# Kernel tuning notes

Hardware: AMD Instinct MI355X
Metric: run time of the kernel (lower is better)

The kernel has to match this reference:

```python
import jax, jax.numpy as jnp
import numpy as np

EPS = 1e-6

def _layernorm(x, g, b):
    mu = jnp.mean(x, axis=-1, keepdims=True)
    var = jnp.mean(jnp.square(x - mu), axis=-1, keepdims=True)
    return (x - mu) * jax.lax.rsqrt(var + EPS) * g + b

def setup_inputs() -> dict:
    key = jax.random.key(0)
    ks = jax.random.split(key, 5)
    B, S, C = 8, 4096, 2048
    M = 2048  # mid_channels must equal channels (norm2 shape constraint)
    x = jax.random.normal(ks[0], (B, S, C), dtype=jnp.float32)
    w1 = jax.random.normal(ks[1], (C, M), dtype=jnp.float32) * (1.0 / np.sqrt(C))
    b1 = jnp.zeros((M,), dtype=jnp.float32)
    w2 = jax.random.normal(ks[2], (M, C), dtype=jnp.float32) * (1.0 / np.sqrt(M))
    b2 = jnp.zeros((C,), dtype=jnp.float32)
    g1 = jnp.ones((C,), dtype=jnp.float32)
    be1 = jnp.zeros((C,), dtype=jnp.float32)
    g2 = jnp.ones((M,), dtype=jnp.float32)
    be2 = jnp.zeros((M,), dtype=jnp.float32)
    return {"x": x, "w1": w1, "b1": b1, "w2": w2, "b2": b2,
            "g1": g1, "be1": be1, "g2": g2, "be2": be2}

def reference(x, w1, b1, w2, b2, g1, be1, g2, be2):
    h = _layernorm(x, g1, be1)
    h = jax.nn.silu(h)
    h = jnp.einsum('bsc,cm->bsm', h, w1) + b1
    h = _layernorm(h, g2, be2)
    h = jax.nn.silu(h)
    # dropout is identity in eval mode
    h = jnp.einsum('bsm,mc->bsc', h, w2) + b2
    return x + h
```

## Files before the change

### kernel.cpp

```cpp
#include <hip/hip_runtime.h>
#include <hip/hip_bf16.h>
#include <stdint.h>

#define NROWS 32768
#define KDIM  2048
#define MDIM  2048

typedef __attribute__((ext_vector_type(8))) __bf16 bf16x8;
typedef __attribute__((ext_vector_type(4))) __bf16 bf16x4;
typedef __attribute__((ext_vector_type(4))) float  f32x4;

__device__ __forceinline__ void gload16(const __bf16* g, __bf16* l) {
    __builtin_amdgcn_global_load_lds(
        (__attribute__((address_space(1))) void*)(g),
        (__attribute__((address_space(3))) void*)(l), 16, 0, 0);
}

__global__ __launch_bounds__(256) void wsplit(const float* __restrict__ W,
                                              __bf16* __restrict__ th,
                                              __bf16* __restrict__ tl) {
    __shared__ float tile[32][33];
    const int bx = blockIdx.x & 63;
    const int by = blockIdx.x >> 6;
    const int tx = threadIdx.x & 31;
    const int ty = threadIdx.x >> 5;
#pragma unroll
    for (int i = 0; i < 32; i += 8)
        tile[ty + i][tx] = W[(size_t)(by * 32 + ty + i) * MDIM + bx * 32 + tx];
    __syncthreads();
#pragma unroll
    for (int i = 0; i < 32; i += 8) {
        const int m = bx * 32 + ty + i;
        const int k = by * 32 + tx;
        const float v = tile[tx][ty + i];
        const __bf16 hb = (__bf16)v;
        const __bf16 lb = (__bf16)(v - (float)hb);
        th[(size_t)m * KDIM + k] = hb;
        tl[(size_t)m * KDIM + k] = lb;
    }
}

__global__ __launch_bounds__(256) void ln_silu(const float* __restrict__ in,
                                               const float* __restrict__ g,
                                               const float* __restrict__ beta,
                                               __bf16* __restrict__ hi) {
    const int row  = blockIdx.x;
    const int tid  = threadIdx.x;
    const int lane = tid & 63;
    const int wv   = tid >> 6;
    const float* rp = in + (size_t)row * KDIM;

    const float4 v0 = ((const float4*)rp)[tid];
    const float4 v1 = ((const float4*)rp)[tid + 256];

    float s = v0.x + v0.y + v0.z + v0.w + v1.x + v1.y + v1.z + v1.w;
    float q = v0.x * v0.x + v0.y * v0.y + v0.z * v0.z + v0.w * v0.w +
              v1.x * v1.x + v1.y * v1.y + v1.z * v1.z + v1.w * v1.w;

#pragma unroll
    for (int off = 32; off > 0; off >>= 1) {
        s += __shfl_xor(s, off, 64);
        q += __shfl_xor(q, off, 64);
    }
    __shared__ float red[8];
    if (lane == 0) { red[wv] = s; red[4 + wv] = q; }
    __syncthreads();
    s = red[0] + red[1] + red[2] + red[3];
    q = red[4] + red[5] + red[6] + red[7];

    const float mu   = s * (1.0f / KDIM);
    const float var  = q * (1.0f / KDIM) - mu * mu;
    const float rstd = rsqrtf(var + 1e-6f);

    auto emit = [&](float4 v, int c0) {
        bf16x4 h4;
        const float xs[4] = {v.x, v.y, v.z, v.w};
#pragma unroll
        for (int j = 0; j < 4; j++) {
            const int c = c0 + j;
            const float t  = (xs[j] - mu) * rstd * g[c] + beta[c];
            const float sv = t / (1.0f + __expf(-t));
            h4[j] = (__bf16)sv;
        }
        *(bf16x4*)(hi + (size_t)row * KDIM + c0) = h4;
    };
    emit(v0, tid * 4);
    emit(v1, 1024 + tid * 4);
}

#define PB   8192
#define BOFF 24576
#define NT   (KDIM / 32)

#define MM(ACC, A_, H_, L_)                                                    \
    ACC = __builtin_amdgcn_mfma_f32_16x16x32_bf16(A_, H_, ACC, 0, 0, 0);       \
    ACC = __builtin_amdgcn_mfma_f32_16x16x32_bf16(A_, L_, ACC, 0, 0, 0)

#define PHASE_PRE()                                                            \
    __builtin_amdgcn_s_barrier();                                              \
    asm volatile("s_waitcnt lgkmcnt(0)" ::: "memory");                         \
    __builtin_amdgcn_sched_barrier(0);                                         \
    __builtin_amdgcn_s_setprio(1)

#define PHASE_POST()                                                           \
    __builtin_amdgcn_s_setprio(0);                                             \
    __builtin_amdgcn_s_barrier()

__global__ __launch_bounds__(512, 2) void gemm8p(
        const __bf16* __restrict__ Ah,
        const __bf16* __restrict__ Bh, const __bf16* __restrict__ Bl,
        const float* __restrict__ bias, const float* __restrict__ res,
        float* __restrict__ out) {
    __shared__ __align__(16) __bf16 lds[57344];

    const int tid  = threadIdx.x;
    const int lane = tid & 63;
    const int wv   = tid >> 6;
    const int wr   = wv >> 2;
    const int wc   = wv & 3;
    const int ml   = lane & 15;
    const int qk   = lane >> 4;

    const int bid = blockIdx.x;
    const int g   = (bid & 7) * 128 + (bid >> 3);
    const int m0  = (g & 127) * 256;
    const int n0  = (g >> 7) * 256;

    const int srow = wv * 16 + (lane >> 2);
    const int scol = ((lane & 3) ^ ((lane >> 3) & 3)) * 8;
    const __bf16* pA0 = Ah + (size_t)(m0 + srow) * KDIM + scol;
    const __bf16* pA1 = Ah + (size_t)(m0 + 128 + srow) * KDIM + scol;
    const __bf16* pH0 = Bh + (size_t)(n0 + srow) * KDIM + scol;
    const __bf16* pH1 = Bh + (size_t)(n0 + 128 + srow) * KDIM + scol;
    const __bf16* pL0 = Bl + (size_t)(n0 + srow) * KDIM + scol;
    const __bf16* pL1 = Bl + (size_t)(n0 + 128 + srow) * KDIM + scol;
    const int ld0 = wv * 512;
    const int ld1 = 4096 + wv * 512;

    const int cofs = (qk ^ ((ml >> 1) & 3)) * 8;
    const int aoff = (wr * 128 + ml) * 32 + cofs;
    const int boff = (wc * 64 + ml) * 32 + cofs;

    f32x4 acc[8][4] = {};

    gload16(pH0, lds + BOFF + ld0);
    gload16(pH1, lds + BOFF + ld1);
    gload16(pL0, lds + BOFF + PB + ld0);
    gload16(pL1, lds + BOFF + PB + ld1);
    gload16(pA0, lds + ld0);
    gload16(pA1, lds + ld1);
    gload16(pA0 + 32, lds + PB + ld0);
    gload16(pA1 + 32, lds + PB + ld1);
    asm volatile("s_waitcnt vmcnt(2)" ::: "memory");
    __builtin_amdgcn_sched_barrier(0);
    __builtin_amdgcn_s_barrier();

    int ta = 0;
    int pa = 2;
    for (int t = 0; t < NT; ++t) {
        __bf16* const aB = lds + ta * PB;
        __bf16* const hB = lds + BOFF + (t & 1) * 2 * PB;
        __bf16* const lB = hB + PB;
        __bf16* const hN = lds + BOFF + ((t + 1) & 1) * 2 * PB;
        const bool pfB = (t + 1) < NT;
        const bool pfA = (t + 2) < NT;
        const int  kB  = (t + 1) * 32;
        const int  kA  = (t + 2) * 32;

        bf16x8 a0, a1, a2, a3, h0, h1, h2, h3, l0, l1, l2, l3;

        a0 = *(const bf16x8*)(aB + aoff);
        a1 = *(const bf16x8*)(aB + aoff + 512);
        a2 = *(const bf16x8*)(aB + aoff + 1024);
        a3 = *(const bf16x8*)(aB + aoff + 1536);
        h0 = *(const bf16x8*)(hB + boff);
        h1 = *(const bf16x8*)(hB + boff + 512);
        l0 = *(const bf16x8*)(lB + boff);
        l1 = *(const bf16x8*)(lB + boff + 512);
        if (pfB) {
            gload16(pH0 + kB, hN + ld0);
            gload16(pH1 + kB, hN + ld1);
        }
        PHASE_PRE();
        MM(acc[0][0], a0, h0, l0); MM(acc[1][0], a1, h0, l0);
        MM(acc[2][0], a2, h0, l0); MM(acc[3][0], a3, h0, l0);
        MM(acc[0][1], a0, h1, l1); MM(acc[1][1], a1, h1, l1);
        MM(acc[2][1], a2, h1, l1); MM(acc[3][1], a3, h1, l1);
        PHASE_POST();

        h2 = *(const bf16x8*)(hB + boff + 1024);
        h3 = *(const bf16x8*)(hB + boff + 1536);
        l2 = *(const bf16x8*)(lB + boff + 1024);
        l3 = *(const bf16x8*)(lB + boff + 1536);
        if (pfB) {
            gload16(pL0 + kB, hN + PB + ld0);
            gload16(pL1 + kB, hN + PB + ld1);
        }
        PHASE_PRE();
        MM(acc[0][2], a0, h2, l2); MM(acc[1][2], a1, h2, l2);
        MM(acc[2][2], a2, h2, l2); MM(acc[3][2], a3, h2, l2);
        MM(acc[0][3], a0, h3, l3); MM(acc[1][3], a1, h3, l3);
        MM(acc[2][3], a2, h3, l3); MM(acc[3][3], a3, h3, l3);
        PHASE_POST();

        a0 = *(const bf16x8*)(aB + aoff + 2048);
        a1 = *(const bf16x8*)(aB + aoff + 2560);
        a2 = *(const bf16x8*)(aB + aoff + 3072);
        a3 = *(const bf16x8*)(aB + aoff + 3584);
        if (pfA) {
            gload16(pA0 + kA, lds + pa * PB + ld0);
            gload16(pA1 + kA, lds + pa * PB + ld1);
        }
        PHASE_PRE();
        MM(acc[4][2], a0, h2, l2); MM(acc[5][2], a1, h2, l2);
        MM(acc[6][2], a2, h2, l2); MM(acc[7][2], a3, h2, l2);
        MM(acc[4][3], a0, h3, l3); MM(acc[5][3], a1, h3, l3);
        MM(acc[6][3], a2, h3, l3); MM(acc[7][3], a3, h3, l3);
        PHASE_POST();

        PHASE_PRE();
        MM(acc[4][0], a0, h0, l0); MM(acc[5][0], a1, h0, l0);
        MM(acc[6][0], a2, h0, l0); MM(acc[7][0], a3, h0, l0);
        MM(acc[4][1], a0, h1, l1); MM(acc[5][1], a1, h1, l1);
        MM(acc[6][1], a2, h1, l1); MM(acc[7][1], a3, h1, l1);
        __builtin_amdgcn_s_setprio(0);
        if (pfA) {
            asm volatile("s_waitcnt vmcnt(2)" ::: "memory");
        } else if (pfB) {
            asm volatile("s_waitcnt vmcnt(0)" ::: "memory");
        }
        __builtin_amdgcn_sched_barrier(0);
        if (pfB) __builtin_amdgcn_s_barrier();

        ta = (ta == 2) ? 0 : ta + 1;
        pa = (pa == 2) ? 0 : pa + 1;
    }

#pragma unroll
    for (int i = 0; i < 8; i++) {
        const int gm = m0 + wr * 128 + (i >> 2) * 64 + (i & 3) * 16 + qk * 4;
#pragma unroll
        for (int j = 0; j < 4; j++) {
            const int gn = n0 + wc * 64 + j * 16 + ml;
            const float bv = bias[gn];
#pragma unroll
            for (int r = 0; r < 4; r++) {
                const size_t idx = (size_t)(gm + r) * MDIM + gn;
                float v = acc[i][j][r] + bv;
                if (res) v += res[idx];
                out[idx] = v;
            }
        }
    }
}

extern "C" void kernel_launch(void* const* d_in, const int* in_sizes, int n_in,
                              void* d_out, int out_size, void* d_ws, size_t ws_size,
                              hipStream_t stream) {
    const float* x   = (const float*)d_in[0];
    const float* w1  = (const float*)d_in[1];
    const float* b1  = (const float*)d_in[2];
    const float* w2  = (const float*)d_in[3];
    const float* b2  = (const float*)d_in[4];
    const float* g1  = (const float*)d_in[5];
    const float* be1 = (const float*)d_in[6];
    const float* g2  = (const float*)d_in[7];
    const float* be2 = (const float*)d_in[8];
    float* out = (float*)d_out;

    char* ws = (char*)d_ws;
    const size_t PLANE = (size_t)NROWS * KDIM * 2;
    const size_t WPL   = (size_t)KDIM * MDIM * 2;
    __bf16* Ahp = (__bf16*)(ws);
    __bf16* B1h = (__bf16*)(ws + PLANE);
    __bf16* B1l = (__bf16*)(ws + PLANE + WPL);
    __bf16* B2h = (__bf16*)(ws + PLANE + 2 * WPL);
    __bf16* B2l = (__bf16*)(ws + PLANE + 3 * WPL);

    wsplit<<<4096, 256, 0, stream>>>(w1, B1h, B1l);
    wsplit<<<4096, 256, 0, stream>>>(w2, B2h, B2l);

    ln_silu<<<NROWS, 256, 0, stream>>>(x, g1, be1, Ahp);
    gemm8p<<<(NROWS / 256) * (MDIM / 256), 512, 0, stream>>>(
        Ahp, B1h, B1l, b1, nullptr, out);

    ln_silu<<<NROWS, 256, 0, stream>>>(out, g2, be2, Ahp);
    gemm8p<<<(NROWS / 256) * (MDIM / 256), 512, 0, stream>>>(
        Ahp, B2h, B2l, b2, x, out);
}
```

Measured before the change: 1.654 ms.

## Replace 8-phase ping-pong GEMM schedule with single-phase load-all-then-compute loop

Removes the four intra-iteration barrier/setprio phases that interleaved LDS fragment reads, global prefetches and MFMA groups. Each K-step now reads all A and B fragments into registers up front, issues every prefetch, then runs all 64 MFMAs under raised priority with a single barrier at the end. This cuts the number of block barriers per iteration, but it raises register pressure and loses the fine-grained overlap between LDS reads and MFMA work across the two co-resident waves.

```diff
diff --git a/kernel.cpp b/kernel.cpp
--- a/kernel.cpp
+++ b/kernel.cpp
@@ -88,7 +88,8 @@
     emit(v1, 1024 + tid * 4);
 }
 
-#define PB   8192
+#define PB_A 8192
+#define PB_B 8192
 #define BOFF 24576
 #define NT   (KDIM / 32)
 
@@ -96,17 +97,7 @@
     ACC = __builtin_amdgcn_mfma_f32_16x16x32_bf16(A_, H_, ACC, 0, 0, 0);       \
     ACC = __builtin_amdgcn_mfma_f32_16x16x32_bf16(A_, L_, ACC, 0, 0, 0)
 
-#define PHASE_PRE()                                                            \
-    __builtin_amdgcn_s_barrier();                                              \
-    asm volatile("s_waitcnt lgkmcnt(0)" ::: "memory");                         \
-    __builtin_amdgcn_sched_barrier(0);                                         \
-    __builtin_amdgcn_s_setprio(1)
-
-#define PHASE_POST()                                                           \
-    __builtin_amdgcn_s_setprio(0);                                             \
-    __builtin_amdgcn_s_barrier()
-
-__global__ __launch_bounds__(512, 2) void gemm8p(
+__global__ __launch_bounds__(512, 2) void gemmtp(
         const __bf16* __restrict__ Ah,
         const __bf16* __restrict__ Bh, const __bf16* __restrict__ Bl,
         const float* __restrict__ bias, const float* __restrict__ res,
@@ -145,95 +136,88 @@
 
     gload16(pH0, lds + BOFF + ld0);
     gload16(pH1, lds + BOFF + ld1);
-    gload16(pL0, lds + BOFF + PB + ld0);
-    gload16(pL1, lds + BOFF + PB + ld1);
+    gload16(pL0, lds + BOFF + PB_B + ld0);
+    gload16(pL1, lds + BOFF + PB_B + ld1);
     gload16(pA0, lds + ld0);
     gload16(pA1, lds + ld1);
-    gload16(pA0 + 32, lds + PB + ld0);
-    gload16(pA1 + 32, lds + PB + ld1);
+    gload16(pA0 + 32, lds + PB_A + ld0);
+    gload16(pA1 + 32, lds + PB_A + ld1);
     asm volatile("s_waitcnt vmcnt(2)" ::: "memory");
     __builtin_amdgcn_sched_barrier(0);
     __builtin_amdgcn_s_barrier();
+    __builtin_amdgcn_sched_barrier(0);
 
     int ta = 0;
-    int pa = 2;
     for (int t = 0; t < NT; ++t) {
-        __bf16* const aB = lds + ta * PB;
-        __bf16* const hB = lds + BOFF + (t & 1) * 2 * PB;
-        __bf16* const lB = hB + PB;
-        __bf16* const hN = lds + BOFF + ((t + 1) & 1) * 2 * PB;
+        __bf16* const aCur = lds + ta * PB_A;
+        const int tan_ = (ta == 2) ? 0 : ta + 1;
+        const int pa_  = (tan_ == 2) ? 0 : tan_ + 1;
+        __bf16* const bCur = lds + BOFF + ((t & 1) ? 2 * PB_B : 0);
+        __bf16* const bNxt = lds + BOFF + ((t & 1) ? 0 : 2 * PB_B);
         const bool pfB = (t + 1) < NT;
         const bool pfA = (t + 2) < NT;
-        const int  kB  = (t + 1) * 32;
-        const int  kA  = (t + 2) * 32;
-
-        bf16x8 a0, a1, a2, a3, h0, h1, h2, h3, l0, l1, l2, l3;
-
-        a0 = *(const bf16x8*)(aB + aoff);
-        a1 = *(const bf16x8*)(aB + aoff + 512);
-        a2 = *(const bf16x8*)(aB + aoff + 1024);
-        a3 = *(const bf16x8*)(aB + aoff + 1536);
-        h0 = *(const bf16x8*)(hB + boff);
-        h1 = *(const bf16x8*)(hB + boff + 512);
-        l0 = *(const bf16x8*)(lB + boff);
-        l1 = *(const bf16x8*)(lB + boff + 512);
+
+        bf16x8 aL[4], aH[4], hB[4], lB[4];
+        aL[0] = *(const bf16x8*)(aCur + aoff);
+        aL[1] = *(const bf16x8*)(aCur + aoff + 512);
+        aL[2] = *(const bf16x8*)(aCur + aoff + 1024);
+        aL[3] = *(const bf16x8*)(aCur + aoff + 1536);
+        hB[0] = *(const bf16x8*)(bCur + boff);
+        hB[1] = *(const bf16x8*)(bCur + boff + 512);
+        hB[2] = *(const bf16x8*)(bCur + boff + 1024);
+        hB[3] = *(const bf16x8*)(bCur + boff + 1536);
+        lB[0] = *(const bf16x8*)(bCur + PB_B + boff);
+        lB[1] = *(const bf16x8*)(bCur + PB_B + boff + 512);
+        lB[2] = *(const bf16x8*)(bCur + PB_B + boff + 1024);
+        lB[3] = *(const bf16x8*)(bCur + PB_B + boff + 1536);
+        aH[0] = *(const bf16x8*)(aCur + aoff + 2048);
+        aH[1] = *(const bf16x8*)(aCur + aoff + 2560);
+        aH[2] = *(const bf16x8*)(aCur + aoff + 3072);
+        aH[3] = *(const bf16x8*)(aCur + aoff + 3584);
+
         if (pfB) {
-            gload16(pH0 + kB, hN + ld0);
-            gload16(pH1 + kB, hN + ld1);
-        }
-        PHASE_PRE();
-        MM(acc[0][0], a0, h0, l0); MM(acc[1][0], a1, h0, l0);
-        MM(acc[2][0], a2, h0, l0); MM(acc[3][0], a3, h0, l0);
-        MM(acc[0][1], a0, h1, l1); MM(acc[1][1], a1, h1, l1);
-        MM(acc[2][1], a2, h1, l1); MM(acc[3][1], a3, h1, l1);
-        PHASE_POST();
-
-        h2 = *(const bf16x8*)(hB + boff + 1024);
-        h3 = *(const bf16x8*)(hB + boff + 1536);
-        l2 = *(const bf16x8*)(lB + boff + 1024);
-        l3 = *(const bf16x8*)(lB + boff + 1536);
-        if (pfB) {
-            gload16(pL0 + kB, hN + PB + ld0);
-            gload16(pL1 + kB, hN + PB + ld1);
-        }
-        PHASE_PRE();
-        MM(acc[0][2], a0, h2, l2); MM(acc[1][2], a1, h2, l2);
-        MM(acc[2][2], a2, h2, l2); MM(acc[3][2], a3, h2, l2);
-        MM(acc[0][3], a0, h3, l3); MM(acc[1][3], a1, h3, l3);
-        MM(acc[2][3], a2, h3, l3); MM(acc[3][3], a3, h3, l3);
-        PHASE_POST();
-
-        a0 = *(const bf16x8*)(aB + aoff + 2048);
-        a1 = *(const bf16x8*)(aB + aoff + 2560);
-        a2 = *(const bf16x8*)(aB + aoff + 3072);
-        a3 = *(const bf16x8*)(aB + aoff + 3584);
+            const int kB = (t + 1) * 32;
+            gload16(pH0 + kB, bNxt + ld0);
+            gload16(pH1 + kB, bNxt + ld1);
+            gload16(pL0 + kB, bNxt + PB_B + ld0);
+            gload16(pL1 + kB, bNxt + PB_B + ld1);
+        }
         if (pfA) {
-            gload16(pA0 + kA, lds + pa * PB + ld0);
-            gload16(pA1 + kA, lds + pa * PB + ld1);
-        }
-        PHASE_PRE();
-        MM(acc[4][2], a0, h2, l2); MM(acc[5][2], a1, h2, l2);
-        MM(acc[6][2], a2, h2, l2); MM(acc[7][2], a3, h2, l2);
-        MM(acc[4][3], a0, h3, l3); MM(acc[5][3], a1, h3, l3);
-        MM(acc[6][3], a2, h3, l3); MM(acc[7][3], a3, h3, l3);
-        PHASE_POST();
-
-        PHASE_PRE();
-        MM(acc[4][0], a0, h0, l0); MM(acc[5][0], a1, h0, l0);
-        MM(acc[6][0], a2, h0, l0); MM(acc[7][0], a3, h0, l0);
-        MM(acc[4][1], a0, h1, l1); MM(acc[5][1], a1, h1, l1);
-        MM(acc[6][1], a2, h1, l1); MM(acc[7][1], a3, h1, l1);
+            const int kA = (t + 2) * 32;
+            gload16(pA0 + kA, lds + pa_ * PB_A + ld0);
+            gload16(pA1 + kA, lds + pa_ * PB_A + ld1);
+        }
+
+        __builtin_amdgcn_s_setprio(1);
+        MM(acc[0][0], aL[0], hB[0], lB[0]); MM(acc[1][0], aL[1], hB[0], lB[0]);
+        MM(acc[2][0], aL[2], hB[0], lB[0]); MM(acc[3][0], aL[3], hB[0], lB[0]);
+        MM(acc[0][1], aL[0], hB[1], lB[1]); MM(acc[1][1], aL[1], hB[1], lB[1]);
+        MM(acc[2][1], aL[2], hB[1], lB[1]); MM(acc[3][1], aL[3], hB[1], lB[1]);
+        MM(acc[0][2], aL[0], hB[2], lB[2]); MM(acc[1][2], aL[1], hB[2], lB[2]);
+        MM(acc[2][2], aL[2], hB[2], lB[2]); MM(acc[3][2], aL[3], hB[2], lB[2]);
+        MM(acc[0][3], aL[0], hB[3], lB[3]); MM(acc[1][3], aL[1], hB[3], lB[3]);
+        MM(acc[2][3], aL[2], hB[3], lB[3]); MM(acc[3][3], aL[3], hB[3], lB[3]);
+        MM(acc[4][0], aH[0], hB[0], lB[0]); MM(acc[5][0], aH[1], hB[0], lB[0]);
+        MM(acc[6][0], aH[2], hB[0], lB[0]); MM(acc[7][0], aH[3], hB[0], lB[0]);
+        MM(acc[4][1], aH[0], hB[1], lB[1]); MM(acc[5][1], aH[1], hB[1], lB[1]);
+        MM(acc[6][1], aH[2], hB[1], lB[1]); MM(acc[7][1], aH[3], hB[1], lB[1]);
+        MM(acc[4][2], aH[0], hB[2], lB[2]); MM(acc[5][2], aH[1], hB[2], lB[2]);
+        MM(acc[6][2], aH[2], hB[2], lB[2]); MM(acc[7][2], aH[3], hB[2], lB[2]);
+        MM(acc[4][3], aH[0], hB[3], lB[3]); MM(acc[5][3], aH[1], hB[3], lB[3]);
+        MM(acc[6][3], aH[2], hB[3], lB[3]); MM(acc[7][3], aH[3], hB[3], lB[3]);
         __builtin_amdgcn_s_setprio(0);
+
         if (pfA) {
             asm volatile("s_waitcnt vmcnt(2)" ::: "memory");
         } else if (pfB) {
             asm volatile("s_waitcnt vmcnt(0)" ::: "memory");
         }
         __builtin_amdgcn_sched_barrier(0);
-        if (pfB) __builtin_amdgcn_s_barrier();
-
-        ta = (ta == 2) ? 0 : ta + 1;
-        pa = (pa == 2) ? 0 : pa + 1;
+        if (pfB) {
+            __builtin_amdgcn_s_barrier();
+            __builtin_amdgcn_sched_barrier(0);
+        }
+        ta = tan_;
     }
 
 #pragma unroll
@@ -281,10 +265,10 @@
     wsplit<<<4096, 256, 0, stream>>>(w2, B2h, B2l);
 
     ln_silu<<<NROWS, 256, 0, stream>>>(x, g1, be1, Ahp);
-    gemm8p<<<(NROWS / 256) * (MDIM / 256), 512, 0, stream>>>(
+    gemmtp<<<(NROWS / 256) * (MDIM / 256), 512, 0, stream>>>(
         Ahp, B1h, B1l, b1, nullptr, out);
 
     ln_silu<<<NROWS, 256, 0, stream>>>(out, g2, be2, Ahp);
-    gemm8p<<<(NROWS / 256) * (MDIM / 256), 512, 0, stream>>>(
+    gemmtp<<<(NROWS / 256) * (MDIM / 256), 512, 0, stream>>>(
         Ahp, B2h, B2l, b2, x, out);
 }
```

Result: no change. 1.632 ms (-1.3%).
